# Performance work log

Measured on AMD Instinct MI355X. Metric: run time of the kernel, lower is better.

## Reference

```python
import jax, jax.numpy as jnp
import numpy as np

H, C = 8, 640            # n_heads, sentence_size (per-head out channels)
HC = H * C               # 5120 concatenated head width
NS, NW, NSEC = 8192, 65536, 1024   # sentences, words, sections
EW, ES, ESEC = 131072, 262144, 16384
WORD, SENT, SECT = 300, 640, 512
FFN_HID = 2048


def setup_inputs() -> dict:
    key = jax.random.key(0)
    ks = jax.random.split(key, 32)
    f = lambda k, sh: (jax.random.normal(k, sh, jnp.float32) * 0.02)
    ri = jax.random.randint
    inp = {}
    inp['Hs'] = jax.random.normal(ks[0], (NS, SENT), jnp.float32)
    inp['Hw'] = jax.random.normal(ks[1], (NW, WORD), jnp.float32)
    inp['HS'] = jax.random.normal(ks[2], (NSEC, SECT), jnp.float32)
    # edge_index convention: row 0 = source nodes, row 1 = target (sentence) nodes
    inp['w2s'] = jnp.stack([ri(ks[3], (EW,), 0, NW), ri(ks[4], (EW,), 0, NS)]).astype(jnp.int32)
    inp['s2s'] = jnp.stack([ri(ks[5], (ES,), 0, NS), ri(ks[6], (ES,), 0, NS)]).astype(jnp.int32)
    inp['S2s'] = jnp.stack([ri(ks[7], (ESEC,), 0, NSEC), ri(ks[8], (ESEC,), 0, NS)]).astype(jnp.int32)
    # gat_w: bipartite (word -> sentence)
    inp['Ww_src'] = f(ks[9], (WORD, HC)); inp['Ww_dst'] = f(ks[10], (SENT, HC))
    inp['aw_src'] = f(ks[11], (H, C)); inp['aw_dst'] = f(ks[12], (H, C)); inp['bw'] = f(ks[13], (HC,))
    # gat_s: sentence -> sentence (shared lin for src/dst)
    inp['Ws'] = f(ks[14], (SENT, HC))
    inp['as_src'] = f(ks[15], (H, C)); inp['as_dst'] = f(ks[16], (H, C)); inp['bs'] = f(ks[17], (HC,))
    # gat_S: bipartite (section -> sentence)
    inp['WS_src'] = f(ks[18], (SECT, HC)); inp['WS_dst'] = f(ks[19], (SENT, HC))
    inp['aS_src'] = f(ks[20], (H, C)); inp['aS_dst'] = f(ks[21], (H, C)); inp['bS'] = f(ks[22], (HC,))
    # fusion gates
    inp['F1_w'] = f(ks[23], (2 * HC, HC)); inp['F1_b'] = f(ks[24], (HC,))
    inp['F2_w'] = f(ks[25], (2 * HC, HC)); inp['F2_b'] = f(ks[26], (HC,))
    # FFN
    inp['l1_w'] = f(ks[27], (HC, FFN_HID)); inp['l1_b'] = f(ks[28], (FFN_HID,))
    inp['l2_w'] = f(ks[29], (FFN_HID, SENT)); inp['l2_b'] = f(ks[30], (SENT,))
    return inp


def _gat(xs, xd, Wsrc, Wdst, asrc, adst, b, edge_index):
    """PyG-style GATConv (concat heads), bipartite (xs -> xd)."""
    N = xd.shape[0]
    hs = (xs @ Wsrc).reshape(-1, H, C)          # [Nsrc,H,C]
    hd = (xd @ Wdst).reshape(-1, H, C)          # [Ndst,H,C]
    al_s = jnp.einsum('nhc,hc->nh', hs, asrc)   # [Nsrc,H]
    al_d = jnp.einsum('nhc,hc->nh', hd, adst)   # [Ndst,H]
    src, dst = edge_index[0], edge_index[1]
    e = jax.nn.leaky_relu(al_s[src] + al_d[dst], negative_slope=0.2)  # [E,H]
    m = jax.ops.segment_max(e, dst, num_segments=N)                   # segment-stable softmax
    ex = jnp.exp(e - m[dst])
    den = jax.ops.segment_sum(ex, dst, num_segments=N)
    alpha = ex / (den[dst] + 1e-16)
    out = jax.ops.segment_sum(hs[src] * alpha[:, :, None], dst, num_segments=N)
    return out.reshape(N, HC) + b


def _fusion(X, Y, W, b):
    Z = jax.nn.sigmoid(jnp.concatenate([X, Y], axis=-1) @ W + b)
    return Z * X + (1.0 - Z) * Y


def reference(Hs, Hw, HS, w2s, s2s, S2s,
              Ww_src, Ww_dst, aw_src, aw_dst, bw,
              Ws, as_src, as_dst, bs,
              WS_src, WS_dst, aS_src, aS_dst, bS,
              F1_w, F1_b, F2_w, F2_b,
              l1_w, l1_b, l2_w, l2_b):
    Uw = jax.nn.elu(_gat(Hw, Hs, Ww_src, Ww_dst, aw_src, aw_dst, bw, w2s))
    Us = jax.nn.elu(_gat(Hs, Hs, Ws, Ws, as_src, as_dst, bs, s2s))
    US = jax.nn.elu(_gat(HS, Hs, WS_src, WS_dst, aS_src, aS_dst, bS, S2s))
    U1 = _fusion(Uw, Us, F1_w, F1_b)
    U2 = _fusion(U1, US, F2_w, F2_b)
    return (U2 @ l1_w + l1_b) @ l2_w + l2_b + Hs
```

## Files before the change

kernel.cpp:

```cpp
#include <hip/hip_runtime.h>
#include <cstdint>
#include <cstddef>

typedef __attribute__((ext_vector_type(8))) __bf16 bf16x8;
typedef __attribute__((ext_vector_type(4))) float f32x4;

static constexpr int kNS   = 8192;
static constexpr int kNW   = 65536;
static constexpr int kNSEC = 1024;
static constexpr int kEW   = 131072;
static constexpr int kES   = 262144;
static constexpr int kESEC = 16384;

__device__ __forceinline__ float eluf(float x)  { return x > 0.f ? x : (__expf(x) - 1.f); }
__device__ __forceinline__ float sigmf(float x) { return 1.f / (1.f + __expf(-x)); }

__device__ __forceinline__ void gload16(const __bf16* g, __bf16* l) {
  __builtin_amdgcn_global_load_lds((const __attribute__((address_space(1))) unsigned int*)g,
                                   (__attribute__((address_space(3))) unsigned int*)l,
                                   16, 0, 0);
}

__global__ __launch_bounds__(256) void conv_transpose(const float* __restrict__ W, int K, int N,
                                                      __bf16* __restrict__ Wt, int KP) {
  __shared__ float t[64][33];
  const int nb = blockIdx.x * 32, kb = blockIdx.y * 64;
  const int tx = threadIdx.x & 31, ty = threadIdx.x >> 5;
#pragma unroll
  for (int i = ty; i < 64; i += 8) {
    const int k = kb + i;
    t[i][tx] = (k < K) ? W[(long)k * N + nb + tx] : 0.f;
  }
  __syncthreads();
  union BU { __bf16 b; unsigned short u; };
#pragma unroll
  for (int i = ty; i < 32; i += 8) {
    BU b0, b1;
    b0.b = (__bf16)t[tx * 2][i];
    b1.b = (__bf16)t[tx * 2 + 1][i];
    const unsigned int pk = ((unsigned int)b1.u << 16) | b0.u;
    *(unsigned int*)(Wt + (long)(nb + i) * KP + kb + tx * 2) = pk;
  }
}

__global__ __launch_bounds__(256) void conv_bf(const float* __restrict__ in, __bf16* __restrict__ outb, long n) {
  long i = (long)blockIdx.x * blockDim.x + threadIdx.x;
  if (i < n) outb[i] = (__bf16)in[i];
}

struct HVJ { const float* W; const float* a; float* o; int Kd; int KP; };
struct HVJobs { HVJ j[6]; };

__global__ __launch_bounds__(256) void head_vecs6(HVJobs jb) {
  const HVJ J = jb.j[blockIdx.z];
  const int h = blockIdx.x;
  const int lane = threadIdx.x & 63;
  const int k = blockIdx.y * 4 + (threadIdx.x >> 6);
  if (k >= J.KP) return;
  float s = 0.f;
  if (k < J.Kd) {
    const float* wr = J.W + (long)k * 5120 + h * 640;
    const float* ar = J.a + h * 640;
    for (int c = lane; c < 640; c += 64) s += wr[c] * ar[c];
  }
  for (int o2 = 32; o2; o2 >>= 1) s += __shfl_down(s, o2);
  if (lane == 0) J.o[h * J.KP + k] = (k < J.Kd) ? s : 0.f;
}

__global__ __launch_bounds__(256) void comb_bias(const float* __restrict__ l1_b, const float* __restrict__ l2_w,
                                                 const float* __restrict__ l2_b, float* __restrict__ bc) {
  const int n = blockIdx.x * 256 + threadIdx.x;
  if (n >= 640) return;
  float s = l2_b[n];
  for (int k = 0; k < 2048; ++k) s += l1_b[k] * l2_w[(long)k * 640 + n];
  bc[n] = s;
}

__global__ __launch_bounds__(256) void att_logits(const float* __restrict__ X, int ldx, int Kd,
                                                  const float* __restrict__ vec, int KP,
                                                  float* __restrict__ outl, int N) {
  const int lane = threadIdx.x & 63;
  const int node = blockIdx.x * 4 + (threadIdx.x >> 6);
  if (node >= N) return;
  const float* xr = X + (long)node * ldx;
  float p[8];
#pragma unroll
  for (int h = 0; h < 8; ++h) p[h] = 0.f;
  for (int k = lane; k < Kd; k += 64) {
    const float xv = xr[k];
#pragma unroll
    for (int h = 0; h < 8; ++h) p[h] += xv * vec[h * KP + k];
  }
#pragma unroll
  for (int h = 0; h < 8; ++h) {
    float v = p[h];
    for (int o2 = 32; o2; o2 >>= 1) v += __shfl_down(v, o2);
    if (lane == 0) outl[(long)node * 8 + h] = v;
  }
}

__global__ __launch_bounds__(256) void att_logits4(const float* __restrict__ X,
                                                   const float* __restrict__ v0, const float* __restrict__ v1,
                                                   const float* __restrict__ v2, const float* __restrict__ v3,
                                                   float* __restrict__ o0, float* __restrict__ o1,
                                                   float* __restrict__ o2, float* __restrict__ o3, int N) {
  const int lane = threadIdx.x & 63;
  const int node = blockIdx.x * 4 + (threadIdx.x >> 6);
  if (node >= N) return;
  const float* xr = X + (long)node * 640;
  float p[4][8];
#pragma unroll
  for (int s = 0; s < 4; ++s)
#pragma unroll
    for (int h = 0; h < 8; ++h) p[s][h] = 0.f;
  for (int k = lane; k < 640; k += 64) {
    const float xv = xr[k];
#pragma unroll
    for (int h = 0; h < 8; ++h) {
      p[0][h] += xv * v0[h * 640 + k];
      p[1][h] += xv * v1[h * 640 + k];
      p[2][h] += xv * v2[h * 640 + k];
      p[3][h] += xv * v3[h * 640 + k];
    }
  }
  float* outs[4] = {o0, o1, o2, o3};
#pragma unroll
  for (int s = 0; s < 4; ++s)
#pragma unroll
    for (int h = 0; h < 8; ++h) {
      float v = p[s][h];
      for (int o2v = 32; o2v; o2v >>= 1) v += __shfl_down(v, o2v);
      if (lane == 0) outs[s][(long)node * 8 + h] = v;
    }
}

__global__ __launch_bounds__(256) void edge_count3(const int* __restrict__ d0, int E0, int* __restrict__ c0,
                                                   const int* __restrict__ d1, int E1, int* __restrict__ c1,
                                                   const int* __restrict__ d2, int E2, int* __restrict__ c2) {
  const int gid = blockIdx.x * blockDim.x + threadIdx.x;
  if (gid < E0) atomicAdd(&c0[d0[gid]], 1);
  else if (gid < E0 + E1) atomicAdd(&c1[d1[gid - E0]], 1);
  else if (gid < E0 + E1 + E2) atomicAdd(&c2[d2[gid - E0 - E1]], 1);
}

__global__ __launch_bounds__(1024) void scan_off3(const int* __restrict__ c0, int* __restrict__ o0,
                                                  const int* __restrict__ c1, int* __restrict__ o1,
                                                  const int* __restrict__ c2, int* __restrict__ o2) {
  const int* cnt = blockIdx.x == 0 ? c0 : (blockIdx.x == 1 ? c1 : c2);
  int* offo = blockIdx.x == 0 ? o0 : (blockIdx.x == 1 ? o1 : o2);
  __shared__ int part[1024];
  const int tid = threadIdx.x;
  const int base = tid * 8;
  int loc[8];
  int s = 0;
#pragma unroll
  for (int i = 0; i < 8; ++i) { loc[i] = s; s += cnt[base + i]; }
  part[tid] = s;
  __syncthreads();
  for (int d2 = 1; d2 < 1024; d2 <<= 1) {
    int v = (tid >= d2) ? part[tid - d2] : 0;
    __syncthreads();
    part[tid] += v;
    __syncthreads();
  }
  const int pre = (tid > 0) ? part[tid - 1] : 0;
#pragma unroll
  for (int i = 0; i < 8; ++i) offo[base + i] = pre + loc[i];
  if (tid == 1023) offo[8192] = part[1023];
}

__global__ __launch_bounds__(256) void edge_fill3(
    const int* __restrict__ s0, const int* __restrict__ d0, int E0, const int* __restrict__ of0, int* __restrict__ cu0, int* __restrict__ sr0,
    const int* __restrict__ s1, const int* __restrict__ d1, int E1, const int* __restrict__ of1, int* __restrict__ cu1, int* __restrict__ sr1,
    const int* __restrict__ s2, const int* __restrict__ d2, int E2, const int* __restrict__ of2, int* __restrict__ cu2, int* __restrict__ sr2) {
  const int gid = blockIdx.x * blockDim.x + threadIdx.x;
  if (gid < E0) {
    const int d = d0[gid];
    sr0[of0[d] + atomicAdd(&cu0[d], 1)] = s0[gid];
  } else if (gid < E0 + E1) {
    const int g = gid - E0, d = d1[g];
    sr1[of1[d] + atomicAdd(&cu1[d], 1)] = s1[g];
  } else if (gid < E0 + E1 + E2) {
    const int g = gid - E0 - E1, d = d2[g];
    sr2[of2[d] + atomicAdd(&cu2[d], 1)] = s2[g];
  }
}

template <int FPAD, int F, bool XPH, bool BIASELU>
__global__ __launch_bounds__(256) void gat_agg(const int* __restrict__ seg_off, const int* __restrict__ ssrc,
                                               const float* __restrict__ als, const float* __restrict__ ald,
                                               const float* __restrict__ X, int ldx,
                                               __bf16* __restrict__ outp, int ldo,
                                               const float* __restrict__ bias) {
  constexpr int C4 = F / 4;
  constexpr int ITEMS = 8 * C4;
  constexpr int L = (ITEMS + 255) / 256;
  const int d = blockIdx.x;
  const int tid = threadIdx.x;
  const int o0 = seg_off[d], o1 = seg_off[d + 1];
  const int deg = o1 - o0;
  __shared__ float exl[64][8];
  __shared__ int ssl[64];
  __shared__ float aldd[8];
  __shared__ float den_s[8];
  if (tid < 8) { aldd[tid] = ald[(long)d * 8 + tid]; den_s[tid] = 0.f; }
  f32x4 acc[L];
  int hh[L], xo[L], oo[L];
  bool vld[L];
#pragma unroll
  for (int l = 0; l < L; ++l) {
    const int idx = tid + l * 256;
    vld[l] = (idx < ITEMS);
    const int h = vld[l] ? (idx / C4) : 0;
    const int c = vld[l] ? (idx - h * C4) : 0;
    hh[l] = h;
    xo[l] = (XPH ? h * F : 0) + c * 4;
    oo[l] = h * FPAD + c * 4;
#pragma unroll
    for (int r = 0; r < 4; ++r) acc[l][r] = 0.f;
  }
  __syncthreads();
  for (int base = 0; base < deg; base += 64) {
    const int nc = min(64, deg - base);
    if (tid < nc) ssl[tid] = ssrc[o0 + base + tid];
    __syncthreads();
    for (int t = tid; t < nc * 8; t += 256) {
      const int e = t >> 3, h = t & 7;
      float v = als[(long)ssl[e] * 8 + h] + aldd[h];
      v = v > 0.f ? v : 0.2f * v;
      exl[e][h] = __expf(v);
    }
    __syncthreads();
    if (tid < 8) {
      float s = 0.f;
      for (int e = 0; e < nc; ++e) s += exl[e][tid];
      den_s[tid] += s;
    }
    for (int e = 0; e < nc; ++e) {
      const float* xr = X + (long)ssl[e] * ldx;
      const float* ex8 = exl[e];
#pragma unroll
      for (int l = 0; l < L; ++l)
        if (vld[l]) {
          const f32x4 v = *(const f32x4*)(xr + xo[l]);
          acc[l] += ex8[hh[l]] * v;
        }
    }
    __syncthreads();
  }
#pragma unroll
  for (int l = 0; l < L; ++l) {
    if (!vld[l]) continue;
    const float dinv = 1.f / (den_s[hh[l]] + 1e-16f);
#pragma unroll
    for (int j = 0; j < 4; ++j) {
      float r = acc[l][j] * dinv;
      if constexpr (BIASELU) { r += bias[oo[l] + j]; r = eluf(r); }
      outp[(long)d * ldo + oo[l] + j] = (__bf16)r;
    }
  }
}

template <int FPAD, int F, bool XPH, bool BIASELU>
__global__ __launch_bounds__(256) void gat_agg_bf(const int* __restrict__ seg_off, const int* __restrict__ ssrc,
                                                  const float* __restrict__ als, const float* __restrict__ ald,
                                                  const __bf16* __restrict__ X, int ldx,
                                                  __bf16* __restrict__ outp, int ldo,
                                                  const float* __restrict__ bias) {
  constexpr int C8 = F / 8;
  constexpr int ITEMS = 8 * C8;
  constexpr int L = (ITEMS + 255) / 256;
  const int d = blockIdx.x;
  const int tid = threadIdx.x;
  const int o0 = seg_off[d], o1 = seg_off[d + 1];
  const int deg = o1 - o0;
  __shared__ float exl[64][8];
  __shared__ int ssl[64];
  __shared__ float aldd[8];
  __shared__ float den_s[8];
  if (tid < 8) { aldd[tid] = ald[(long)d * 8 + tid]; den_s[tid] = 0.f; }
  float acc[L][8];
  int hh[L], xo[L], oo[L];
  bool vld[L];
#pragma unroll
  for (int l = 0; l < L; ++l) {
    const int idx = tid + l * 256;
    vld[l] = (idx < ITEMS);
    const int h = vld[l] ? (idx / C8) : 0;
    const int c = vld[l] ? (idx - h * C8) : 0;
    hh[l] = h;
    xo[l] = (XPH ? h * F : 0) + c * 8;
    oo[l] = h * FPAD + c * 8;
#pragma unroll
    for (int r = 0; r < 8; ++r) acc[l][r] = 0.f;
  }
  __syncthreads();
  for (int base = 0; base < deg; base += 64) {
    const int nc = min(64, deg - base);
    if (tid < nc) ssl[tid] = ssrc[o0 + base + tid];
    __syncthreads();
    for (int t = tid; t < nc * 8; t += 256) {
      const int e = t >> 3, h = t & 7;
      float v = als[(long)ssl[e] * 8 + h] + aldd[h];
      v = v > 0.f ? v : 0.2f * v;
      exl[e][h] = __expf(v);
    }
    __syncthreads();
    if (tid < 8) {
      float s = 0.f;
      for (int e = 0; e < nc; ++e) s += exl[e][tid];
      den_s[tid] += s;
    }
    for (int e = 0; e < nc; ++e) {
      const __bf16* xr = X + (long)ssl[e] * ldx;
      const float* ex8 = exl[e];
#pragma unroll
      for (int l = 0; l < L; ++l)
        if (vld[l]) {
          const bf16x8 v = *(const bf16x8*)(xr + xo[l]);
          const float w = ex8[hh[l]];
#pragma unroll
          for (int r = 0; r < 8; ++r) acc[l][r] += w * (float)v[r];
        }
    }
    __syncthreads();
  }
#pragma unroll
  for (int l = 0; l < L; ++l) {
    if (!vld[l]) continue;
    const float dinv = 1.f / (den_s[hh[l]] + 1e-16f);
#pragma unroll
    for (int j = 0; j < 8; ++j) {
      float r = acc[l][j] * dinv;
      if constexpr (BIASELU) { r += bias[oo[l] + j]; r = eluf(r); }
      outp[(long)d * ldo + oo[l] + j] = (__bf16)r;
    }
  }
}

template <int EPI>
__global__ __launch_bounds__(256) void gemm_bt(
    const __bf16* __restrict__ A, int lda, const __bf16* __restrict__ A2, int ksplit,
    const __bf16* __restrict__ Bt, int ldb, int K,
    void* __restrict__ Cout, int ldc,
    const float* __restrict__ bias,
    const __bf16* __restrict__ Xg, const __bf16* __restrict__ Yg, int ldxy,
    const float* __restrict__ Res, int ldres,
    long a_zs, long bt_zs, long c_zs, int b_zs) {
  __shared__ __bf16 sA[2][128 * 32];
  __shared__ __bf16 sB[2][128 * 32];
  const int tid = threadIdx.x;
  const int z = blockIdx.z;
  const int m0 = blockIdx.y * 128, n0 = blockIdx.x * 128;
  const __bf16* Ab = A + (long)z * a_zs;
  const __bf16* A2b = A2 ? A2 + (long)z * a_zs : nullptr;
  const __bf16* Btb = Bt + (long)z * bt_zs;
  const int lane = tid & 63;
  const int wv = tid >> 6, wr = wv >> 1, wc = wv & 1;
  const int fr = lane & 15, fq = lane >> 4;

  const int r0 = tid >> 2, r1 = r0 + 64;
  const int csw = (((tid & 3) ^ ((r0 >> 1) & 3)) * 8);
  const int ldst0 = tid * 8;
  const int ldst1 = 2048 + tid * 8;

  f32x4 acc[4][4];
#pragma unroll
  for (int i = 0; i < 4; ++i)
#pragma unroll
    for (int j = 0; j < 4; ++j)
#pragma unroll
      for (int r = 0; r < 4; ++r) acc[i][j][r] = 0.f;

  const int fsw = (fq ^ ((fr >> 1) & 3)) * 8;
  int aof[4], bof[4];
#pragma unroll
  for (int i = 0; i < 4; ++i) {
    aof[i] = (wr * 64 + i * 16 + fr) * 32 + fsw;
    bof[i] = (wc * 64 + i * 16 + fr) * 32 + fsw;
  }

  const int nkt = K >> 5;
  auto stage = [&](int buf, int kt) {
    const int k0 = kt * 32;
    const __bf16* As = Ab;
    int kr = k0;
    if (A2b && k0 >= ksplit) { As = A2b; kr = k0 - ksplit; }
    gload16(As + (long)(m0 + r0) * lda + kr + csw, &sA[buf][ldst0]);
    gload16(As + (long)(m0 + r1) * lda + kr + csw, &sA[buf][ldst1]);
    gload16(Btb + (long)(n0 + r0) * ldb + k0 + csw, &sB[buf][ldst0]);
    gload16(Btb + (long)(n0 + r1) * ldb + k0 + csw, &sB[buf][ldst1]);
  };

  stage(0, 0);
  for (int kt = 0; kt < nkt; ++kt) {
    const int cur = kt & 1;
    __syncthreads();
    if (kt + 1 < nkt) stage(cur ^ 1, kt + 1);
    bf16x8 af[4], bfv[4];
#pragma unroll
    for (int i = 0; i < 4; ++i) {
      af[i] = *(const bf16x8*)(&sA[cur][aof[i]]);
      bfv[i] = *(const bf16x8*)(&sB[cur][bof[i]]);
    }
#pragma unroll
    for (int i = 0; i < 4; ++i)
#pragma unroll
      for (int j = 0; j < 4; ++j)
        acc[i][j] = __builtin_amdgcn_mfma_f32_16x16x32_bf16(af[i], bfv[j], acc[i][j], 0, 0, 0);
  }

  const float* biasb = bias ? bias + (long)z * b_zs : nullptr;
#pragma unroll
  for (int i = 0; i < 4; ++i) {
#pragma unroll
    for (int j = 0; j < 4; ++j) {
#pragma unroll
      for (int r = 0; r < 4; ++r) {
        const int mm = m0 + wr * 64 + i * 16 + fq * 4 + r;
        const int nn = n0 + wc * 64 + j * 16 + fr;
        const float v = acc[i][j][r];
        const long cidx = (long)mm * ldc + nn + (long)z * c_zs;
        if constexpr (EPI == 0) {
          ((float*)Cout)[cidx] = v;
        } else if constexpr (EPI == 1) {
          ((__bf16*)Cout)[cidx] = (__bf16)eluf(v + biasb[nn]);
        } else if constexpr (EPI == 2) {
          const float zt = sigmf(v + biasb[nn]);
          const float x = (float)Xg[(long)mm * ldxy + nn];
          const float y = (float)Yg[(long)mm * ldxy + nn];
          ((__bf16*)Cout)[cidx] = (__bf16)(zt * x + (1.f - zt) * y);
        } else if constexpr (EPI == 3) {
          ((__bf16*)Cout)[cidx] = (__bf16)(v + biasb[nn]);
        } else if constexpr (EPI == 4) {
          ((float*)Cout)[cidx] = v + biasb[nn] + Res[(long)mm * ldres + nn];
        } else {
          ((__bf16*)Cout)[cidx] = (__bf16)v;
        }
      }
    }
  }
}

template <int EPI>
__global__ __launch_bounds__(512, 2) void gemm256(
    const __bf16* __restrict__ A, int lda, const __bf16* __restrict__ A2, int ksplit,
    const __bf16* __restrict__ Bt, int ldb, int K,
    void* __restrict__ Cout, int ldc,
    const float* __restrict__ bias,
    const __bf16* __restrict__ Xg, const __bf16* __restrict__ Yg, int ldxy,
    int nn_tiles, int ngemm,
    const float* __restrict__ tW, __bf16* __restrict__ tWt, int tK, int tN, int tKP) {
  __shared__ __bf16 sA[2][2][256 * 32];
  __shared__ __bf16 sB[2][2][256 * 32];
  const int tid = threadIdx.x;
  const int lin = blockIdx.x;

  if (lin >= ngemm) {
    if (tW) {
      float* sc = (float*)&sA[0][0][0];
      const int nworkers = gridDim.x - ngemm;
      const int wid = lin - ngemm;
      const int ntx = tN >> 5, nty = tKP >> 6;
      const int tx = tid & 31, ty = tid >> 5;
      union BU { __bf16 b; unsigned short u; };
      for (int tile = wid; tile < ntx * nty; tile += nworkers) {
        const int nb = (tile % ntx) * 32, kb = (tile / ntx) * 64;
#pragma unroll
        for (int i = ty; i < 64; i += 16) {
          const int k = kb + i;
          sc[i * 33 + tx] = (k < tK) ? tW[(long)k * tN + nb + tx] : 0.f;
        }
        __syncthreads();
#pragma unroll
        for (int i = ty; i < 32; i += 16) {
          BU b0, b1;
          b0.b = (__bf16)sc[(tx * 2) * 33 + i];
          b1.b = (__bf16)sc[(tx * 2 + 1) * 33 + i];
          const unsigned int pk = ((unsigned int)b1.u << 16) | b0.u;
          *(unsigned int*)(tWt + (long)(nb + i) * tKP + kb + tx * 2) = pk;
        }
        __syncthreads();
      }
    }
    return;
  }

  const int nwg = ngemm;
  const int qq = nwg >> 3, rr = nwg & 7;
  const int xcd = lin & 7, pos = lin >> 3;
  const int swz = (xcd < rr ? xcd * (qq + 1) : rr * (qq + 1) + (xcd - rr) * qq) + pos;
  const int m0 = (swz / nn_tiles) * 256;
  const int n0 = (swz % nn_tiles) * 256;

  const int lane = tid & 63;
  const int wv = tid >> 6, wm = wv >> 2, wn = wv & 3;
  const int fr = lane & 15, fq = lane >> 4;

  const int srow = tid >> 2;
  const int pslot = tid & 3;

  auto stageA = [&](int bp, int tt, int kk) {
    const int kcol0 = tt * 64 + kk * 32;
    const __bf16* src = A;
    int kc = kcol0;
    if (A2 && kcol0 >= ksplit) { src = A2; kc = kcol0 - ksplit; }
    __bf16* dst = &sA[bp][kk][0];
#pragma unroll
    for (int i = 0; i < 2; ++i) {
      const int r = i * 128 + srow;
      const int l = pslot ^ ((r >> 1) & 3);
      gload16(src + (long)(m0 + r) * lda + kc + l * 8, dst + (i * 512 + tid) * 8);
    }
  };
  auto stageB = [&](int bp, int tt, int kk) {
    const int kcol0 = tt * 64 + kk * 32;
    __bf16* dst = &sB[bp][kk][0];
#pragma unroll
    for (int i = 0; i < 2; ++i) {
      const int r = i * 128 + srow;
      const int l = pslot ^ ((r >> 1) & 3);
      gload16(Bt + (long)(n0 + r) * ldb + kcol0 + l * 8, dst + (i * 512 + tid) * 8);
    }
  };

  int aoff[8], boff[4];
#pragma unroll
  for (int mf = 0; mf < 8; ++mf) {
    const int ra = wm * 128 + mf * 16 + fr;
    aoff[mf] = ra * 32 + ((fq ^ ((ra >> 1) & 3)) * 8);
  }
#pragma unroll
  for (int nf = 0; nf < 4; ++nf) {
    const int rb = wn * 64 + nf * 16 + fr;
    boff[nf] = rb * 32 + ((fq ^ ((rb >> 1) & 3)) * 8);
  }

  f32x4 acc[8][4];
#pragma unroll
  for (int i = 0; i < 8; ++i)
#pragma unroll
    for (int j = 0; j < 4; ++j)
#pragma unroll
      for (int r = 0; r < 4; ++r) acc[i][j][r] = 0.f;

  const int nkt = K >> 6;

  bf16x8 aA[4], aB[4], bA[4], bB[4];

  stageA(0, 0, 0); stageB(0, 0, 0); stageA(0, 0, 1); stageB(0, 0, 1);
  asm volatile("s_waitcnt vmcnt(4)" ::: "memory");
  __builtin_amdgcn_s_barrier();
#pragma unroll
  for (int mf = 0; mf < 4; ++mf) aA[mf] = *(const bf16x8*)(&sA[0][0][aoff[mf]]);
#pragma unroll
  for (int nf = 0; nf < 4; ++nf) bA[nf] = *(const bf16x8*)(&sB[0][0][boff[nf]]);

  for (int t = 0; t < nkt; ++t) {
    const int cb = t & 1, nb = cb ^ 1;
    const bool pf = (t + 1 < nkt);

#pragma unroll
    for (int mf = 0; mf < 4; ++mf) aB[mf] = *(const bf16x8*)(&sA[cb][0][aoff[4 + mf]]);
    if (pf) stageA(nb, t + 1, 0);
    asm volatile("s_waitcnt lgkmcnt(4)" ::: "memory");
    __builtin_amdgcn_sched_barrier(0);
    __builtin_amdgcn_s_setprio(1);
#pragma unroll
    for (int mf = 0; mf < 4; ++mf)
#pragma unroll
      for (int nf = 0; nf < 4; ++nf)
        acc[mf][nf] = __builtin_amdgcn_mfma_f32_16x16x32_bf16(aA[mf], bA[nf], acc[mf][nf], 0, 0, 0);
    __builtin_amdgcn_s_setprio(0);
    __builtin_amdgcn_sched_barrier(0);

    if (pf) stageB(nb, t + 1, 0);
    if (pf) asm volatile("s_waitcnt vmcnt(4)" ::: "memory");
    else    asm volatile("s_waitcnt vmcnt(0)" ::: "memory");
    __builtin_amdgcn_s_barrier();

#pragma unroll
    for (int mf = 0; mf < 4; ++mf) aA[mf] = *(const bf16x8*)(&sA[cb][1][aoff[mf]]);
#pragma unroll
    for (int nf = 0; nf < 4; ++nf) bB[nf] = *(const bf16x8*)(&sB[cb][1][boff[nf]]);
    asm volatile("s_waitcnt lgkmcnt(8)" ::: "memory");
    __builtin_amdgcn_sched_barrier(0);
    __builtin_amdgcn_s_setprio(1);
#pragma unroll
    for (int mf = 0; mf < 4; ++mf)
#pragma unroll
      for (int nf = 0; nf < 4; ++nf)
        acc[4 + mf][nf] = __builtin_amdgcn_mfma_f32_16x16x32_bf16(aB[mf], bA[nf], acc[4 + mf][nf], 0, 0, 0);
    __builtin_amdgcn_s_setprio(0);
    __builtin_amdgcn_sched_barrier(0);

#pragma unroll
    for (int mf = 0; mf < 4; ++mf) aB[mf] = *(const bf16x8*)(&sA[cb][1][aoff[4 + mf]]);
    if (pf) stageA(nb, t + 1, 1);
    asm volatile("s_waitcnt lgkmcnt(4)" ::: "memory");
    __builtin_amdgcn_sched_barrier(0);
    __builtin_amdgcn_s_setprio(1);
#pragma unroll
    for (int mf = 0; mf < 4; ++mf)
#pragma unroll
      for (int nf = 0; nf < 4; ++nf)
        acc[mf][nf] = __builtin_amdgcn_mfma_f32_16x16x32_bf16(aA[mf], bB[nf], acc[mf][nf], 0, 0, 0);
    __builtin_amdgcn_s_setprio(0);
    __builtin_amdgcn_sched_barrier(0);

    if (pf) {
      stageB(nb, t + 1, 1);
      asm volatile("s_waitcnt vmcnt(4)" ::: "memory");
    }
    __builtin_amdgcn_s_barrier();

    if (pf) {
#pragma unroll
      for (int mf = 0; mf < 4; ++mf) aA[mf] = *(const bf16x8*)(&sA[nb][0][aoff[mf]]);
#pragma unroll
      for (int nf = 0; nf < 4; ++nf) bA[nf] = *(const bf16x8*)(&sB[nb][0][boff[nf]]);
      asm volatile("s_waitcnt lgkmcnt(8)" ::: "memory");
    } else {
      asm volatile("s_waitcnt lgkmcnt(0)" ::: "memory");
    }
    __builtin_amdgcn_sched_barrier(0);
    __builtin_amdgcn_s_setprio(1);
#pragma unroll
    for (int mf = 0; mf < 4; ++mf)
#pragma unroll
      for (int nf = 0; nf < 4; ++nf)
        acc[4 + mf][nf] = __builtin_amdgcn_mfma_f32_16x16x32_bf16(aB[mf], bB[nf], acc[4 + mf][nf], 0, 0, 0);
    __builtin_amdgcn_s_setprio(0);
    __builtin_amdgcn_sched_barrier(0);
  }

#pragma unroll
  for (int mf = 0; mf < 8; ++mf) {
#pragma unroll
    for (int nf = 0; nf < 4; ++nf) {
#pragma unroll
      for (int r = 0; r < 4; ++r) {
        const int mm = m0 + wm * 128 + mf * 16 + fq * 4 + r;
        const int nn = n0 + wn * 64 + nf * 16 + fr;
        const float v = acc[mf][nf][r];
        const long cidx = (long)mm * ldc + nn;
        if constexpr (EPI == 2) {
          const float zt = sigmf(v + bias[nn]);
          const float x = (float)Xg[(long)mm * ldxy + nn];
          const float y = (float)Yg[(long)mm * ldxy + nn];
          ((__bf16*)Cout)[cidx] = (__bf16)(zt * x + (1.f - zt) * y);
        } else {
          ((__bf16*)Cout)[cidx] = (__bf16)(v + bias[nn]);
        }
      }
    }
  }
}

extern "C" void kernel_launch(void* const* d_in, const int* in_sizes, int n_in,
                              void* d_out, int out_size, void* d_ws, size_t ws_size,
                              hipStream_t stream) {
  (void)in_sizes; (void)n_in; (void)out_size;
  const float* Hs    = (const float*)d_in[0];
  const float* Hw    = (const float*)d_in[1];
  const float* HSec  = (const float*)d_in[2];
  const int* w2s     = (const int*)d_in[3];
  const int* s2s     = (const int*)d_in[4];
  const int* S2s     = (const int*)d_in[5];
  const float* Ww_src = (const float*)d_in[6];
  const float* Ww_dst = (const float*)d_in[7];
  const float* aw_src = (const float*)d_in[8];
  const float* aw_dst = (const float*)d_in[9];
  const float* bw     = (const float*)d_in[10];
  const float* Wss    = (const float*)d_in[11];
  const float* as_src = (const float*)d_in[12];
  const float* as_dst = (const float*)d_in[13];
  const float* bs     = (const float*)d_in[14];
  const float* WS_src = (const float*)d_in[15];
  const float* WS_dst = (const float*)d_in[16];
  const float* aS_src = (const float*)d_in[17];
  const float* aS_dst = (const float*)d_in[18];
  const float* bS     = (const float*)d_in[19];
  const float* F1_w   = (const float*)d_in[20];
  const float* F1_b   = (const float*)d_in[21];
  const float* F2_w   = (const float*)d_in[22];
  const float* F2_b   = (const float*)d_in[23];
  const float* l1_w   = (const float*)d_in[24];
  const float* l1_b   = (const float*)d_in[25];
  const float* l2_w   = (const float*)d_in[26];
  const float* l2_b   = (const float*)d_in[27];
  float* outp = (float*)d_out;

  char* ws = (char*)d_ws;
  size_t cur_off = 0;
  auto alloc = [&](size_t bytes) -> char* {
    char* p = ws + cur_off;
    cur_off = (cur_off + bytes + 255) & ~(size_t)255;
    return p;
  };

  __bf16* Wt_w  = (__bf16*)alloc((size_t)5120 * 320 * 2);
  __bf16* Wt_s  = (__bf16*)alloc((size_t)5120 * 640 * 2);
  __bf16* Wt_S  = (__bf16*)alloc((size_t)5120 * 512 * 2);
  __bf16* WtF   = (__bf16*)alloc((size_t)5120 * 10240 * 2);
  __bf16* Wt_l2 = (__bf16*)alloc((size_t)640 * 2048 * 2);
  __bf16* l1_bf = (__bf16*)alloc((size_t)5120 * 2048 * 2);
  __bf16* WcT   = (__bf16*)alloc((size_t)640 * 5120 * 2);
  float*  bc    = (float*)alloc(640 * 4);
  __bf16* HS_bf = (__bf16*)alloc((size_t)1024 * 512 * 2);
  __bf16* Hs_bf = (__bf16*)alloc((size_t)kNS * 640 * 2);
  float* v_w = (float*)alloc(8 * 320 * 4);
  float* u_w = (float*)alloc(8 * 640 * 4);
  float* v_s = (float*)alloc(8 * 640 * 4);
  float* u_s = (float*)alloc(8 * 640 * 4);
  float* v_S = (float*)alloc(8 * 512 * 4);
  float* u_S = (float*)alloc(8 * 640 * 4);
  float* alw_s = (float*)alloc((size_t)kNW * 8 * 4);
  float* alw_d = (float*)alloc((size_t)kNS * 8 * 4);
  float* als_s = (float*)alloc((size_t)kNS * 8 * 4);
  float* als_d = (float*)alloc((size_t)kNS * 8 * 4);
  float* alS_s = (float*)alloc((size_t)kNSEC * 8 * 4);
  float* alS_d = (float*)alloc((size_t)kNS * 8 * 4);
  int* csr_i  = (int*)alloc((size_t)6 * kNS * 4);
  int* cnt_w = csr_i, *cnt_s = csr_i + kNS, *cnt_S = csr_i + 2 * kNS;
  int* cur_w = csr_i + 3 * kNS, *cur_s = csr_i + 4 * kNS, *cur_S = csr_i + 5 * kNS;
  int* off_w = (int*)alloc((size_t)(kNS + 1) * 4);
  int* off_s = (int*)alloc((size_t)(kNS + 1) * 4);
  int* off_S = (int*)alloc((size_t)(kNS + 1) * 4);
  int* ssrc_w = (int*)alloc((size_t)kEW * 4);
  int* ssrc_s = (int*)alloc((size_t)kES * 4);
  int* ssrc_S = (int*)alloc((size_t)kESEC * 4);
  __bf16* hs_Sb = (__bf16*)alloc((size_t)1024 * 5120 * 2);
  char* aggreg = alloc((size_t)kNS * 2560 * 2 + (size_t)kNS * 5120 * 2);
  __bf16* agg_w = (__bf16*)aggreg;
  __bf16* agg_s = (__bf16*)(aggreg + (size_t)kNS * 2560 * 2);
  __bf16* U1 = (__bf16*)aggreg;
  __bf16* Uw = (__bf16*)alloc((size_t)kNS * 5120 * 2);
  __bf16* Us = (__bf16*)alloc((size_t)kNS * 5120 * 2);
  __bf16* US = (__bf16*)alloc((size_t)kNS * 5120 * 2);
  __bf16* U2 = Uw;

  __bf16* WtF2 = nullptr;
  {
    const size_t f2b = (size_t)5120 * 10240 * 2;
    if (cur_off + f2b + 256 <= ws_size) WtF2 = (__bf16*)alloc(f2b);
  }

  const dim3 b256(256);

  conv_transpose<<<dim3(160, 5), b256, 0, stream>>>(Ww_src, 300, 5120, Wt_w, 320);
  conv_transpose<<<dim3(160, 10), b256, 0, stream>>>(Wss, 640, 5120, Wt_s, 640);
  conv_transpose<<<dim3(160, 8), b256, 0, stream>>>(WS_src, 512, 5120, Wt_S, 512);
  conv_transpose<<<dim3(160, 160), b256, 0, stream>>>(F1_w, 10240, 5120, WtF, 10240);
  conv_transpose<<<dim3(20, 32), b256, 0, stream>>>(l2_w, 2048, 640, Wt_l2, 2048);
  conv_bf<<<(1024 * 512 + 255) / 256, b256, 0, stream>>>(HSec, HS_bf, (long)1024 * 512);
  conv_bf<<<((long)kNS * 640 + 255) / 256, b256, 0, stream>>>(Hs, Hs_bf, (long)kNS * 640);
  conv_bf<<<((long)5120 * 2048 + 255) / 256, b256, 0, stream>>>(l1_w, l1_bf, (long)5120 * 2048);

  gemm_bt<5><<<dim3(40, 5, 1), b256, 0, stream>>>(
      Wt_l2, 2048, nullptr, 1 << 30, l1_bf, 2048, 2048,
      WcT, 5120, nullptr, nullptr, nullptr, 0, nullptr, 0, 0, 0, 0, 0);
  comb_bias<<<3, b256, 0, stream>>>(l1_b, l2_w, l2_b, bc);

  {
    HVJobs jb;
    jb.j[0] = {Ww_src, aw_src, v_w, 300, 320};
    jb.j[1] = {Ww_dst, aw_dst, u_w, 640, 640};
    jb.j[2] = {Wss,    as_src, v_s, 640, 640};
    jb.j[3] = {Wss,    as_dst, u_s, 640, 640};
    jb.j[4] = {WS_src, aS_src, v_S, 512, 512};
    jb.j[5] = {WS_dst, aS_dst, u_S, 640, 640};
    head_vecs6<<<dim3(8, 160, 6), b256, 0, stream>>>(jb);
  }

  att_logits<<<(kNW + 3) / 4, b256, 0, stream>>>(Hw, 300, 300, v_w, 320, alw_s, kNW);
  att_logits<<<(kNSEC + 3) / 4, b256, 0, stream>>>(HSec, 512, 512, v_S, 512, alS_s, kNSEC);
  att_logits4<<<(kNS + 3) / 4, b256, 0, stream>>>(Hs, u_w, v_s, u_s, u_S,
                                                  alw_d, als_s, als_d, alS_d, kNS);

  hipMemsetAsync(csr_i, 0, (size_t)6 * kNS * 4, stream);
  edge_count3<<<(kEW + kES + kESEC + 255) / 256, b256, 0, stream>>>(
      w2s + kEW, kEW, cnt_w, s2s + kES, kES, cnt_s, S2s + kESEC, kESEC, cnt_S);
  scan_off3<<<3, 1024, 0, stream>>>(cnt_w, off_w, cnt_s, off_s, cnt_S, off_S);
  edge_fill3<<<(kEW + kES + kESEC + 255) / 256, b256, 0, stream>>>(
      w2s, w2s + kEW, kEW, off_w, cur_w, ssrc_w,
      s2s, s2s + kES, kES, off_s, cur_s, ssrc_s,
      S2s, S2s + kESEC, kESEC, off_S, cur_S, ssrc_S);

  gemm_bt<5><<<dim3(40, 8, 1), b256, 0, stream>>>(
      HS_bf, 512, nullptr, 1 << 30, Wt_S, 512, 512,
      hs_Sb, 5120, nullptr, nullptr, nullptr, 0, nullptr, 0, 0, 0, 0, 0);

  gat_agg<320, 300, false, false><<<kNS, b256, 0, stream>>>(off_w, ssrc_w, alw_s, alw_d, Hw, 300, agg_w, 2560, nullptr);
  gat_agg_bf<640, 640, false, false><<<kNS, b256, 0, stream>>>(off_s, ssrc_s, als_s, als_d, Hs_bf, 640, agg_s, 5120, nullptr);
  gat_agg_bf<640, 640, true, true><<<kNS, b256, 0, stream>>>(off_S, ssrc_S, alS_s, alS_d, hs_Sb, 5120, US, 5120, bS);

  gemm_bt<1><<<dim3(5, 64, 8), b256, 0, stream>>>(
      agg_w, 2560, nullptr, 1 << 30, Wt_w, 320, 320,
      Uw, 5120, bw, nullptr, nullptr, 0, nullptr, 0, 320, (long)640 * 320, 640, 640);
  gemm_bt<1><<<dim3(5, 64, 8), b256, 0, stream>>>(
      agg_s, 5120, nullptr, 1 << 30, Wt_s, 640, 640,
      Us, 5120, bs, nullptr, nullptr, 0, nullptr, 0, 640, (long)640 * 640, 640, 640);

  if (WtF2) {
    gemm256<2><<<dim3(640 + 128), dim3(512), 0, stream>>>(
        Uw, 5120, Us, 5120, WtF, 10240, 10240,
        U1, 5120, F1_b, Uw, Us, 5120, 20,
        640, F2_w, WtF2, 10240, 5120, 10240);
  } else {
    gemm256<2><<<dim3(640), dim3(512), 0, stream>>>(
        Uw, 5120, Us, 5120, WtF, 10240, 10240,
        U1, 5120, F1_b, Uw, Us, 5120, 20,
        640, nullptr, nullptr, 0, 0, 0);
    conv_transpose<<<dim3(160, 160), b256, 0, stream>>>(F2_w, 10240, 5120, WtF, 10240);
  }

  gemm256<2><<<dim3(640), dim3(512), 0, stream>>>(
      U1, 5120, US, 5120, WtF2 ? WtF2 : WtF, 10240, 10240,
      U2, 5120, F2_b, U1, US, 5120, 20,
      640, nullptr, nullptr, 0, 0, 0);

  gemm_bt<4><<<dim3(5, 64, 1), b256, 0, stream>>>(
      U2, 5120, nullptr, 1 << 30, WcT, 5120, 5120,
      outp, 640, bc, nullptr, nullptr, 0, Hs, 640, 0, 0, 0, 0);
}
```

Measured before the change: 3.090 ms.

## Switch gemm256 to 32x32x16 MFMA and drop fused F2 weight transpose

The 256x256 fusion-gate GEMM moves from 16x16x32 to 32x32x16 bf16 MFMA tiles. Each wave now holds 4x2 f32x16 accumulators, with LDS fragment offsets and the epilogue row/column mapping changed to match. The path that fused the F2 weight transpose into extra workgroups of the first fusion GEMM is removed; F2_w is now always transposed by a separate conv_transpose launch into the reused WtF buffer. The larger MFMA shape is meant to cut LDS fragment reads per FLOP and the instruction count, but the transpose now runs serially instead of overlapping with the first GEMM.

```diff
diff --git a/kernel.cpp b/kernel.cpp
--- a/kernel.cpp
+++ b/kernel.cpp
@@ -4,6 +4,7 @@
 
 typedef __attribute__((ext_vector_type(8))) __bf16 bf16x8;
 typedef __attribute__((ext_vector_type(4))) float f32x4;
+typedef __attribute__((ext_vector_type(16))) float f32x16;
 
 static constexpr int kNS   = 8192;
 static constexpr int kNW   = 65536;
@@ -449,44 +450,13 @@
     void* __restrict__ Cout, int ldc,
     const float* __restrict__ bias,
     const __bf16* __restrict__ Xg, const __bf16* __restrict__ Yg, int ldxy,
-    int nn_tiles, int ngemm,
-    const float* __restrict__ tW, __bf16* __restrict__ tWt, int tK, int tN, int tKP) {
+    int nn_tiles) {
   __shared__ __bf16 sA[2][2][256 * 32];
   __shared__ __bf16 sB[2][2][256 * 32];
   const int tid = threadIdx.x;
+
+  const int nwg = gridDim.x;
   const int lin = blockIdx.x;
-
-  if (lin >= ngemm) {
-    if (tW) {
-      float* sc = (float*)&sA[0][0][0];
-      const int nworkers = gridDim.x - ngemm;
-      const int wid = lin - ngemm;
-      const int ntx = tN >> 5, nty = tKP >> 6;
-      const int tx = tid & 31, ty = tid >> 5;
-      union BU { __bf16 b; unsigned short u; };
-      for (int tile = wid; tile < ntx * nty; tile += nworkers) {
-        const int nb = (tile % ntx) * 32, kb = (tile / ntx) * 64;
-#pragma unroll
-        for (int i = ty; i < 64; i += 16) {
-          const int k = kb + i;
-          sc[i * 33 + tx] = (k < tK) ? tW[(long)k * tN + nb + tx] : 0.f;
-        }
-        __syncthreads();
-#pragma unroll
-        for (int i = ty; i < 32; i += 16) {
-          BU b0, b1;
-          b0.b = (__bf16)sc[(tx * 2) * 33 + i];
-          b1.b = (__bf16)sc[(tx * 2 + 1) * 33 + i];
-          const unsigned int pk = ((unsigned int)b1.u << 16) | b0.u;
-          *(unsigned int*)(tWt + (long)(nb + i) * tKP + kb + tx * 2) = pk;
-        }
-        __syncthreads();
-      }
-    }
-    return;
-  }
-
-  const int nwg = ngemm;
   const int qq = nwg >> 3, rr = nwg & 7;
   const int xcd = lin & 7, pos = lin >> 3;
   const int swz = (xcd < rr ? xcd * (qq + 1) : rr * (qq + 1) + (xcd - rr) * qq) + pos;
@@ -495,7 +465,8 @@
 
   const int lane = tid & 63;
   const int wv = tid >> 6, wm = wv >> 2, wn = wv & 3;
-  const int fr = lane & 15, fq = lane >> 4;
+  const int lr = lane & 31;
+  const int l5 = lane >> 5;
 
   const int srow = tid >> 2;
   const int pslot = tid & 3;
@@ -524,53 +495,67 @@
     }
   };
 
-  int aoff[8], boff[4];
-#pragma unroll
-  for (int mf = 0; mf < 8; ++mf) {
-    const int ra = wm * 128 + mf * 16 + fr;
-    aoff[mf] = ra * 32 + ((fq ^ ((ra >> 1) & 3)) * 8);
-  }
-#pragma unroll
-  for (int nf = 0; nf < 4; ++nf) {
-    const int rb = wn * 64 + nf * 16 + fr;
-    boff[nf] = rb * 32 + ((fq ^ ((rb >> 1) & 3)) * 8);
-  }
-
-  f32x4 acc[8][4];
-#pragma unroll
-  for (int i = 0; i < 8; ++i)
-#pragma unroll
-    for (int j = 0; j < 4; ++j)
-#pragma unroll
-      for (int r = 0; r < 4; ++r) acc[i][j][r] = 0.f;
+  int aoff[4][2], boff[2][2];
+#pragma unroll
+  for (int mf = 0; mf < 4; ++mf) {
+#pragma unroll
+    for (int s = 0; s < 2; ++s) {
+      const int ra = wm * 128 + mf * 32 + lr;
+      aoff[mf][s] = ra * 32 + (((s * 2 + l5) ^ ((ra >> 1) & 3)) * 8);
+    }
+  }
+#pragma unroll
+  for (int nf = 0; nf < 2; ++nf) {
+#pragma unroll
+    for (int s = 0; s < 2; ++s) {
+      const int rb = wn * 64 + nf * 32 + lr;
+      boff[nf][s] = rb * 32 + (((s * 2 + l5) ^ ((rb >> 1) & 3)) * 8);
+    }
+  }
+
+  f32x16 acc[4][2];
+#pragma unroll
+  for (int i = 0; i < 4; ++i)
+#pragma unroll
+    for (int j = 0; j < 2; ++j)
+#pragma unroll
+      for (int r = 0; r < 16; ++r) acc[i][j][r] = 0.f;
 
   const int nkt = K >> 6;
 
-  bf16x8 aA[4], aB[4], bA[4], bB[4];
+  bf16x8 aA[2][2], aB[2][2], bA[2][2], bB[2][2];
 
   stageA(0, 0, 0); stageB(0, 0, 0); stageA(0, 0, 1); stageB(0, 0, 1);
   asm volatile("s_waitcnt vmcnt(4)" ::: "memory");
   __builtin_amdgcn_s_barrier();
 #pragma unroll
-  for (int mf = 0; mf < 4; ++mf) aA[mf] = *(const bf16x8*)(&sA[0][0][aoff[mf]]);
-#pragma unroll
-  for (int nf = 0; nf < 4; ++nf) bA[nf] = *(const bf16x8*)(&sB[0][0][boff[nf]]);
+  for (int m = 0; m < 2; ++m)
+#pragma unroll
+    for (int s = 0; s < 2; ++s) aA[m][s] = *(const bf16x8*)(&sA[0][0][aoff[m][s]]);
+#pragma unroll
+  for (int n = 0; n < 2; ++n)
+#pragma unroll
+    for (int s = 0; s < 2; ++s) bA[n][s] = *(const bf16x8*)(&sB[0][0][boff[n][s]]);
 
   for (int t = 0; t < nkt; ++t) {
     const int cb = t & 1, nb = cb ^ 1;
     const bool pf = (t + 1 < nkt);
 
 #pragma unroll
-    for (int mf = 0; mf < 4; ++mf) aB[mf] = *(const bf16x8*)(&sA[cb][0][aoff[4 + mf]]);
+    for (int m = 0; m < 2; ++m)
+#pragma unroll
+      for (int s = 0; s < 2; ++s) aB[m][s] = *(const bf16x8*)(&sA[cb][0][aoff[2 + m][s]]);
     if (pf) stageA(nb, t + 1, 0);
     asm volatile("s_waitcnt lgkmcnt(4)" ::: "memory");
     __builtin_amdgcn_sched_barrier(0);
     __builtin_amdgcn_s_setprio(1);
 #pragma unroll
-    for (int mf = 0; mf < 4; ++mf)
-#pragma unroll
-      for (int nf = 0; nf < 4; ++nf)
-        acc[mf][nf] = __builtin_amdgcn_mfma_f32_16x16x32_bf16(aA[mf], bA[nf], acc[mf][nf], 0, 0, 0);
+    for (int m = 0; m < 2; ++m)
+#pragma unroll
+      for (int n = 0; n < 2; ++n)
+#pragma unroll
+        for (int s = 0; s < 2; ++s)
+          acc[m][n] = __builtin_amdgcn_mfma_f32_32x32x16_bf16(aA[m][s], bA[n][s], acc[m][n], 0, 0, 0);
     __builtin_amdgcn_s_setprio(0);
     __builtin_amdgcn_sched_barrier(0);
 
@@ -580,31 +565,41 @@
     __builtin_amdgcn_s_barrier();
 
 #pragma unroll
-    for (int mf = 0; mf < 4; ++mf) aA[mf] = *(const bf16x8*)(&sA[cb][1][aoff[mf]]);
-#pragma unroll
-    for (int nf = 0; nf < 4; ++nf) bB[nf] = *(const bf16x8*)(&sB[cb][1][boff[nf]]);
+    for (int m = 0; m < 2; ++m)
+#pragma unroll
+      for (int s = 0; s < 2; ++s) aA[m][s] = *(const bf16x8*)(&sA[cb][1][aoff[m][s]]);
+#pragma unroll
+    for (int n = 0; n < 2; ++n)
+#pragma unroll
+      for (int s = 0; s < 2; ++s) bB[n][s] = *(const bf16x8*)(&sB[cb][1][boff[n][s]]);
     asm volatile("s_waitcnt lgkmcnt(8)" ::: "memory");
     __builtin_amdgcn_sched_barrier(0);
     __builtin_amdgcn_s_setprio(1);
 #pragma unroll
-    for (int mf = 0; mf < 4; ++mf)
-#pragma unroll
-      for (int nf = 0; nf < 4; ++nf)
-        acc[4 + mf][nf] = __builtin_amdgcn_mfma_f32_16x16x32_bf16(aB[mf], bA[nf], acc[4 + mf][nf], 0, 0, 0);
+    for (int m = 0; m < 2; ++m)
+#pragma unroll
+      for (int n = 0; n < 2; ++n)
+#pragma unroll
+        for (int s = 0; s < 2; ++s)
+          acc[2 + m][n] = __builtin_amdgcn_mfma_f32_32x32x16_bf16(aB[m][s], bA[n][s], acc[2 + m][n], 0, 0, 0);
     __builtin_amdgcn_s_setprio(0);
     __builtin_amdgcn_sched_barrier(0);
 
 #pragma unroll
-    for (int mf = 0; mf < 4; ++mf) aB[mf] = *(const bf16x8*)(&sA[cb][1][aoff[4 + mf]]);
+    for (int m = 0; m < 2; ++m)
+#pragma unroll
+      for (int s = 0; s < 2; ++s) aB[m][s] = *(const bf16x8*)(&sA[cb][1][aoff[2 + m][s]]);
     if (pf) stageA(nb, t + 1, 1);
     asm volatile("s_waitcnt lgkmcnt(4)" ::: "memory");
     __builtin_amdgcn_sched_barrier(0);
     __builtin_amdgcn_s_setprio(1);
 #pragma unroll
-    for (int mf = 0; mf < 4; ++mf)
-#pragma unroll
-      for (int nf = 0; nf < 4; ++nf)
-        acc[mf][nf] = __builtin_amdgcn_mfma_f32_16x16x32_bf16(aA[mf], bB[nf], acc[mf][nf], 0, 0, 0);
+    for (int m = 0; m < 2; ++m)
+#pragma unroll
+      for (int n = 0; n < 2; ++n)
+#pragma unroll
+        for (int s = 0; s < 2; ++s)
+          acc[m][n] = __builtin_amdgcn_mfma_f32_32x32x16_bf16(aA[m][s], bB[n][s], acc[m][n], 0, 0, 0);
     __builtin_amdgcn_s_setprio(0);
     __builtin_amdgcn_sched_barrier(0);
 
@@ -616,9 +611,13 @@
 
     if (pf) {
 #pragma unroll
-      for (int mf = 0; mf < 4; ++mf) aA[mf] = *(const bf16x8*)(&sA[nb][0][aoff[mf]]);
-#pragma unroll
-      for (int nf = 0; nf < 4; ++nf) bA[nf] = *(const bf16x8*)(&sB[nb][0][boff[nf]]);
+      for (int m = 0; m < 2; ++m)
+#pragma unroll
+        for (int s = 0; s < 2; ++s) aA[m][s] = *(const bf16x8*)(&sA[nb][0][aoff[m][s]]);
+#pragma unroll
+      for (int n = 0; n < 2; ++n)
+#pragma unroll
+        for (int s = 0; s < 2; ++s) bA[n][s] = *(const bf16x8*)(&sB[nb][0][boff[n][s]]);
       asm volatile("s_waitcnt lgkmcnt(8)" ::: "memory");
     } else {
       asm volatile("s_waitcnt lgkmcnt(0)" ::: "memory");
@@ -626,22 +625,24 @@
     __builtin_amdgcn_sched_barrier(0);
     __builtin_amdgcn_s_setprio(1);
 #pragma unroll
-    for (int mf = 0; mf < 4; ++mf)
-#pragma unroll
-      for (int nf = 0; nf < 4; ++nf)
-        acc[4 + mf][nf] = __builtin_amdgcn_mfma_f32_16x16x32_bf16(aB[mf], bB[nf], acc[4 + mf][nf], 0, 0, 0);
+    for (int m = 0; m < 2; ++m)
+#pragma unroll
+      for (int n = 0; n < 2; ++n)
+#pragma unroll
+        for (int s = 0; s < 2; ++s)
+          acc[2 + m][n] = __builtin_amdgcn_mfma_f32_32x32x16_bf16(aB[m][s], bB[n][s], acc[2 + m][n], 0, 0, 0);
     __builtin_amdgcn_s_setprio(0);
     __builtin_amdgcn_sched_barrier(0);
   }
 
 #pragma unroll
-  for (int mf = 0; mf < 8; ++mf) {
-#pragma unroll
-    for (int nf = 0; nf < 4; ++nf) {
-#pragma unroll
-      for (int r = 0; r < 4; ++r) {
-        const int mm = m0 + wm * 128 + mf * 16 + fq * 4 + r;
-        const int nn = n0 + wn * 64 + nf * 16 + fr;
+  for (int mf = 0; mf < 4; ++mf) {
+#pragma unroll
+    for (int nf = 0; nf < 2; ++nf) {
+#pragma unroll
+      for (int r = 0; r < 16; ++r) {
+        const int mm = m0 + wm * 128 + mf * 32 + (r & 3) + 8 * (r >> 2) + 4 * l5;
+        const int nn = n0 + wn * 64 + nf * 32 + lr;
         const float v = acc[mf][nf][r];
         const long cidx = (long)mm * ldc + nn;
         if constexpr (EPI == 2) {
@@ -660,7 +661,7 @@
 extern "C" void kernel_launch(void* const* d_in, const int* in_sizes, int n_in,
                               void* d_out, int out_size, void* d_ws, size_t ws_size,
                               hipStream_t stream) {
-  (void)in_sizes; (void)n_in; (void)out_size;
+  (void)in_sizes; (void)n_in; (void)out_size; (void)ws_size;
   const float* Hs    = (const float*)d_in[0];
   const float* Hw    = (const float*)d_in[1];
   const float* HSec  = (const float*)d_in[2];
@@ -740,12 +741,6 @@
   __bf16* US = (__bf16*)alloc((size_t)kNS * 5120 * 2);
   __bf16* U2 = Uw;
 
-  __bf16* WtF2 = nullptr;
-  {
-    const size_t f2b = (size_t)5120 * 10240 * 2;
-    if (cur_off + f2b + 256 <= ws_size) WtF2 = (__bf16*)alloc(f2b);
-  }
-
   const dim3 b256(256);
 
   conv_transpose<<<dim3(160, 5), b256, 0, stream>>>(Ww_src, 300, 5120, Wt_w, 320);
@@ -802,23 +797,14 @@
       agg_s, 5120, nullptr, 1 << 30, Wt_s, 640, 640,
       Us, 5120, bs, nullptr, nullptr, 0, nullptr, 0, 640, (long)640 * 640, 640, 640);
 
-  if (WtF2) {
-    gemm256<2><<<dim3(640 + 128), dim3(512), 0, stream>>>(
-        Uw, 5120, Us, 5120, WtF, 10240, 10240,
-        U1, 5120, F1_b, Uw, Us, 5120, 20,
-        640, F2_w, WtF2, 10240, 5120, 10240);
-  } else {
-    gemm256<2><<<dim3(640), dim3(512), 0, stream>>>(
-        Uw, 5120, Us, 5120, WtF, 10240, 10240,
-        U1, 5120, F1_b, Uw, Us, 5120, 20,
-        640, nullptr, nullptr, 0, 0, 0);
-    conv_transpose<<<dim3(160, 160), b256, 0, stream>>>(F2_w, 10240, 5120, WtF, 10240);
-  }
-
   gemm256<2><<<dim3(640), dim3(512), 0, stream>>>(
-      U1, 5120, US, 5120, WtF2 ? WtF2 : WtF, 10240, 10240,
-      U2, 5120, F2_b, U1, US, 5120, 20,
-      640, nullptr, nullptr, 0, 0, 0);
+      Uw, 5120, Us, 5120, WtF, 10240, 10240,
+      U1, 5120, F1_b, Uw, Us, 5120, 20);
+
+  conv_transpose<<<dim3(160, 160), b256, 0, stream>>>(F2_w, 10240, 5120, WtF, 10240);
+  gemm256<2><<<dim3(640), dim3(512), 0, stream>>>(
+      U1, 5120, US, 5120, WtF, 10240, 10240,
+      U2, 5120, F2_b, U1, US, 5120, 20);
 
   gemm_bt<4><<<dim3(5, 64, 1), b256, 0, stream>>>(
       U2, 5120, nullptr, 1 << 30, WcT, 5120, 5120,
```

After: 3.088 ms. No clear change (-0.1%).
